# Optimization experiments

Measured on AMD Instinct MI355X. Metric: run time of the kernel, lower is better.

Reference implementation:

```python
import jax, jax.numpy as jnp
import numpy as np
from jax import lax

N_QUBITS = 10
Q_DEPTH = 3


def setup_inputs():
    k = jax.random.split(jax.random.key(0), 12)
    B = 2048
    return {
        "x": jax.random.normal(k[0], (B, 1, 28, 28), jnp.float32),
        "conv1_w": jax.random.normal(k[1], (16, 1, 3, 3), jnp.float32) * 0.2,
        "conv1_b": jnp.zeros((16,), jnp.float32),
        "bn1_g": jnp.ones((16,), jnp.float32),
        "bn1_b": jnp.zeros((16,), jnp.float32),
        "conv2_w": jax.random.normal(k[2], (32, 16, 3, 3), jnp.float32) * 0.1,
        "conv2_b": jnp.zeros((32,), jnp.float32),
        "bn2_g": jnp.ones((32,), jnp.float32),
        "bn2_b": jnp.zeros((32,), jnp.float32),
        "fc1_w": jax.random.normal(k[3], (784, 1568), jnp.float32) * 0.01,
        "fc1_b": jnp.zeros((784,), jnp.float32),
        "sel_w": jax.random.normal(k[4], (N_QUBITS, 784), jnp.float32) * 0.01,
        "sel_b": jnp.zeros((N_QUBITS,), jnp.float32),
        "q_params": 0.5 * jax.random.normal(k[5], (Q_DEPTH, N_QUBITS), jnp.float32),
        "post1_w": jax.random.normal(k[6], (32, N_QUBITS), jnp.float32) * 0.01,
        "post1_b": jnp.zeros((32,), jnp.float32),
        "post2_w": jax.random.normal(k[7], (10, 32), jnp.float32) * 0.01,
        "post2_b": jnp.zeros((10,), jnp.float32),
    }


def _conv(x, w, b):
    y = lax.conv_general_dilated(x, w, (1, 1), "SAME",
                                 dimension_numbers=("NCHW", "OIHW", "NCHW"))
    return y + b[None, :, None, None]


def _bn(x, g, b, eps=1e-5):
    # training-mode batch norm (batch statistics), as in the torch module's forward
    m = x.mean((0, 2, 3), keepdims=True)
    v = ((x - m) ** 2).mean((0, 2, 3), keepdims=True)
    return g[None, :, None, None] * (x - m) * lax.rsqrt(v + eps) + b[None, :, None, None]


def _maxpool2(x):
    return lax.reduce_window(x, -jnp.inf, lax.max, (1, 1, 2, 2), (1, 1, 2, 2), "VALID")


def _apply_ry(state, theta, wire):
    # state: real statevector shaped (2,)*N_QUBITS (RY/CZ keep amplitudes real)
    st = jnp.moveaxis(state, wire, 0)
    c, s = jnp.cos(theta / 2), jnp.sin(theta / 2)
    new = jnp.stack([c * st[0] - s * st[1], s * st[0] + c * st[1]])
    return jnp.moveaxis(new, 0, wire)


def _apply_cz(state, wire):
    st = jnp.moveaxis(state, (wire, wire + 1), (0, 1))
    st = st.at[1, 1].multiply(-1.0)
    return jnp.moveaxis(st, (0, 1), (wire, wire + 1))


def _circuit(feats, qw):
    # angle encoding + q_depth x (RY layer, linear CZ chain); returns <Z_i> per qubit
    state = jnp.zeros((2,) * N_QUBITS, feats.dtype).at[(0,) * N_QUBITS].set(1.0)
    for i in range(N_QUBITS):
        state = _apply_ry(state, feats[i] * jnp.pi, i)
    for layer in range(Q_DEPTH):
        for i in range(N_QUBITS):
            state = _apply_ry(state, qw[layer, i], i)
        for i in range(N_QUBITS - 1):
            state = _apply_cz(state, i)
    probs = state * state
    zs = []
    for i in range(N_QUBITS):
        p = jnp.moveaxis(probs, i, 0).reshape(2, -1).sum(1)
        zs.append(p[0] - p[1])
    return jnp.stack(zs)


def reference(x, conv1_w, conv1_b, bn1_g, bn1_b, conv2_w, conv2_b, bn2_g, bn2_b,
              fc1_w, fc1_b, sel_w, sel_b, q_params, post1_w, post1_b, post2_w, post2_b):
    h = _maxpool2(jax.nn.relu(_bn(_conv(x, conv1_w, conv1_b), bn1_g, bn1_b)))   # [B,16,14,14]
    h = _maxpool2(jax.nn.relu(_bn(_conv(h, conv2_w, conv2_b), bn2_g, bn2_b)))   # [B,32,7,7]
    h = h.reshape(h.shape[0], -1)                                               # [B,1568]
    feats = jnp.tanh(h @ fc1_w.T + fc1_b)                                       # [B,784]
    sel = feats @ sel_w.T + sel_b                                               # [B,10]
    q_out = jax.vmap(_circuit, in_axes=(0, None))(sel, q_params)                # [B,10]
    h2 = jax.nn.relu(q_out @ post1_w.T + post1_b)
    return h2 @ post2_w.T + post2_b
```

## Files before the change

kernel.cpp:

```cpp
#include <hip/hip_runtime.h>
#include <math.h>


#define BATCH 2048
#define PI_F 3.14159265358979323846f
#define KP 3328
#define KQ 13
#define BSTR2 312
#define AROW 392
#define APLANE 6272
#define AIMG 12544

typedef unsigned short ushort_t;
typedef __attribute__((ext_vector_type(8))) short bf16x8;
typedef __attribute__((ext_vector_type(4))) float f32x4;

__device__ __forceinline__ float wave_reduce_add(float v) {
#pragma unroll
  for (int off = 32; off >= 1; off >>= 1) v += __shfl_xor(v, off, 64);
  return v;
}

__device__ __forceinline__ ushort_t f2bf(float v) {
  unsigned u = __float_as_uint(v);
  u += 0x7FFFu + ((u >> 16) & 1u);
  return (ushort_t)(u >> 16);
}
__device__ __forceinline__ float bf2f(ushort_t b) {
  return __uint_as_float(((unsigned)b) << 16);
}

__device__ __forceinline__ float tanh_fast(float x) {
  float e = __expf(-2.f * fabsf(x));
  float r = (1.f - e) / (1.f + e);
  return copysignf(r, x);
}

__global__ __launch_bounds__(256) void k_conv1_stats(
    const float* __restrict__ x, const float* __restrict__ cw,
    const float* __restrict__ cb, float* __restrict__ part1,
    const float* __restrict__ cw2, ushort_t* __restrict__ wB,
    const float* __restrict__ fc1w, ushort_t* __restrict__ Bp) {
  const int t = threadIdx.x;
  if (blockIdx.x >= BATCH) {
    const int bid = blockIdx.x - BATCH;
    if (bid == 0) {
      for (int i = t; i < 32 * BSTR2; i += 256) {
        int oc = i / BSTR2, k = i - oc * BSTR2;
        ushort_t val = 0;
        if (k < 288) {
          int sec2 = k >> 4, ic = k & 15;
          if (sec2 < 9) {
            val = f2bf(cw2[oc * 144 + ic * 9 + sec2]);
          } else {
            float w = cw2[oc * 144 + ic * 9 + (sec2 - 9)];
            val = f2bf(w - bf2f(f2bf(w)));
          }
        }
        wB[i] = val;
      }
    } else {
      const int rb = (bid - 1) * 8;
      for (int i = t; i < 8 * (KP / 8); i += 256) {
        int rr = i / (KP / 8), c = i - rr * (KP / 8);
        int n = rb + rr;
        union { ushort_t u[8]; uint4 v; } o;
        o.v = make_uint4(0, 0, 0, 0);
        if (n < 784 && c < 392) {
          int cc = c < 196 ? c : c - 196;
          const float* wp = fc1w + (size_t)n * 1568 + cc * 8;
#pragma unroll
          for (int j = 0; j < 8; ++j) o.u[j] = f2bf(wp[j]);
        }
        ((uint4*)(Bp + (size_t)n * KP))[c] = o.v;
      }
    }
    return;
  }
  const int b = blockIdx.x;
  __shared__ float xs[30][33];
  __shared__ float ws[160];
  __shared__ float redS[16][28];
  __shared__ float redQ[16][28];
  for (int i = t; i < 30 * 33; i += 256) (&xs[0][0])[i] = 0.f;
  if (t < 144) ws[t] = cw[t];
  else if (t < 160) ws[t] = cb[t - 144];
  __syncthreads();
  const float* xb = x + b * 784;
  for (int i = t; i < 784; i += 256) xs[1 + i / 28][1 + (i % 28)] = xb[i];
  __syncthreads();
  for (int task = t; task < 448; task += 256) {
    const int oc = task / 28;
    const int row = task - oc * 28;
    float wk[9];
#pragma unroll
    for (int k = 0; k < 9; ++k) wk[k] = ws[oc * 9 + k];
    const float bc = ws[144 + oc];
    float A0 = xs[row][0], A1 = xs[row][1];
    float B0 = xs[row + 1][0], B1 = xs[row + 1][1];
    float C0 = xs[row + 2][0], C1 = xs[row + 2][1];
    float s = 0.f, q = 0.f;
#pragma unroll 4
    for (int xx = 0; xx < 28; ++xx) {
      float A2 = xs[row][xx + 2], B2 = xs[row + 1][xx + 2], C2 = xs[row + 2][xx + 2];
      float acc = bc;
      acc = fmaf(wk[0], A0, acc); acc = fmaf(wk[1], A1, acc); acc = fmaf(wk[2], A2, acc);
      acc = fmaf(wk[3], B0, acc); acc = fmaf(wk[4], B1, acc); acc = fmaf(wk[5], B2, acc);
      acc = fmaf(wk[6], C0, acc); acc = fmaf(wk[7], C1, acc); acc = fmaf(wk[8], C2, acc);
      s += acc; q = fmaf(acc, acc, q);
      A0 = A1; A1 = A2; B0 = B1; B1 = B2; C0 = C1; C1 = C2;
    }
    redS[oc][row] = s;
    redQ[oc][row] = q;
  }
  __syncthreads();
  if (t < 32) {
    const int c = t >> 1;
    float acc = 0.f;
    if (t & 1) {
#pragma unroll 4
      for (int r = 0; r < 28; ++r) acc += redQ[c][r];
    } else {
#pragma unroll 4
      for (int r = 0; r < 28; ++r) acc += redS[c][r];
    }
    part1[b * 32 + t] = acc;
  }
}

__global__ __launch_bounds__(256) void k_bnstat(
    const float* __restrict__ part, const float* __restrict__ g,
    const float* __restrict__ bb, float* __restrict__ stats,
    int nch, int nblk, double invN) {
  const int c = blockIdx.x;
  const int t = threadIdx.x;
  const int stride = nch * 2;
  double ls = 0.0, lq = 0.0;
  for (int i = t; i < nblk; i += 256) {
    ls += (double)part[i * stride + c * 2];
    lq += (double)part[i * stride + c * 2 + 1];
  }
#pragma unroll
  for (int off = 32; off >= 1; off >>= 1) {
    ls += __shfl_xor(ls, off, 64);
    lq += __shfl_xor(lq, off, 64);
  }
  __shared__ double rs[4], rq[4];
  if ((t & 63) == 0) { rs[t >> 6] = ls; rq[t >> 6] = lq; }
  __syncthreads();
  if (t == 0) {
    double S = rs[0] + rs[1] + rs[2] + rs[3];
    double Q = rq[0] + rq[1] + rq[2] + rq[3];
    double mean = S * invN;
    double var = Q * invN - mean * mean;
    double inv = 1.0 / sqrt(var + 1e-5);
    double sc = (double)g[c] * inv;
    stats[c * 2] = (float)sc;
    stats[c * 2 + 1] = (float)((double)bb[c] - mean * sc);
  }
}

__global__ __launch_bounds__(512, 2) void k_conv2_mfma(
    const float* __restrict__ x, const float* __restrict__ cw1,
    const float* __restrict__ cb1, const float* __restrict__ stats1,
    const ushort_t* __restrict__ wB, const float* __restrict__ cb,
    const float* __restrict__ g2, float* __restrict__ part2,
    float* __restrict__ pooled) {
  const int b0 = blockIdx.x * 2;
  const int t = threadIdx.x;
  __shared__ __align__(16) ushort_t aT[2 * AIMG];
  __shared__ __align__(16) ushort_t bS[32 * BSTR2];
  __shared__ float xs[2][30][33];
  __shared__ float wsc[160];
  __shared__ float red[2][4][64];
  {
    uint4 z = make_uint4(0, 0, 0, 0);
    uint4* a4 = (uint4*)aT;
    for (int i = t; i < (2 * AIMG) / 8; i += 512) a4[i] = z;
    float4* xz = (float4*)&xs[0][0][0];
    if (t < 495) xz[t] = make_float4(0.f, 0.f, 0.f, 0.f);
    if (t < 160) wsc[t] = (t < 144) ? cw1[t] : cb1[t - 144];
    uint4* b4 = (uint4*)bS;
    const uint4* w4 = (const uint4*)wB;
    for (int i = t; i < (32 * BSTR2) / 8; i += 512) b4[i] = w4[i];
  }
  __syncthreads();
  {
    const float* xb = x + (size_t)b0 * 784;
    for (int i = t; i < 1568; i += 512) {
      int img = i / 784, j = i - img * 784;
      xs[img][1 + j / 28][1 + (j % 28)] = xb[img * 784 + j];
    }
  }
  __syncthreads();
  if (t < 448) {
    const int img = t / 224, tt = t - img * 224;
    const int oc = tt / 14, pr = tt - oc * 14;
    float wk[9];
#pragma unroll
    for (int k = 0; k < 9; ++k) wk[k] = wsc[oc * 9 + k];
    const float bc = wsc[144 + oc];
    const float scale = stats1[oc * 2], shift = stats1[oc * 2 + 1];
    const int r0 = 2 * pr;
    float A0 = xs[img][r0][0],     A1 = xs[img][r0][1];
    float B0 = xs[img][r0 + 1][0], B1 = xs[img][r0 + 1][1];
    float C0 = xs[img][r0 + 2][0], C1 = xs[img][r0 + 2][1];
    float D0 = xs[img][r0 + 3][0], D1 = xs[img][r0 + 3][1];
    float pmax = 0.f;
#pragma unroll 4
    for (int xx = 0; xx < 28; ++xx) {
      float A2 = xs[img][r0][xx + 2], B2 = xs[img][r0 + 1][xx + 2];
      float C2 = xs[img][r0 + 2][xx + 2], D2 = xs[img][r0 + 3][xx + 2];
      float c0 = bc, c1 = bc;
      c0 = fmaf(wk[0], A0, c0); c0 = fmaf(wk[1], A1, c0); c0 = fmaf(wk[2], A2, c0);
      c0 = fmaf(wk[3], B0, c0); c0 = fmaf(wk[4], B1, c0); c0 = fmaf(wk[5], B2, c0);
      c0 = fmaf(wk[6], C0, c0); c0 = fmaf(wk[7], C1, c0); c0 = fmaf(wk[8], C2, c0);
      c1 = fmaf(wk[0], B0, c1); c1 = fmaf(wk[1], B1, c1); c1 = fmaf(wk[2], B2, c1);
      c1 = fmaf(wk[3], C0, c1); c1 = fmaf(wk[4], C1, c1); c1 = fmaf(wk[5], C2, c1);
      c1 = fmaf(wk[6], D0, c1); c1 = fmaf(wk[7], D1, c1); c1 = fmaf(wk[8], D2, c1);
      float e0 = fmaxf(fmaf(scale, c0, shift), 0.f);
      float e1 = fmaxf(fmaf(scale, c1, shift), 0.f);
      float m = fmaxf(e0, e1);
      if ((xx & 1) == 0) {
        pmax = m;
      } else {
        float pv = fmaxf(pmax, m);
        ushort_t hi = f2bf(pv);
        ushort_t lo = f2bf(pv - bf2f(hi));
        int off = img * AIMG + (pr + 1) * AROW + ((xx >> 1) + 1) * 24 + oc;
        aT[off] = hi;
        aT[off + APLANE] = lo;
      }
      A0 = A1; A1 = A2; B0 = B1; B1 = B2; C0 = C1; C1 = C2; D0 = D1; D1 = D2;
    }
  }
  __syncthreads();

  const int lane = t & 63;
  const int wv = t >> 6;
  const int img = wv >> 2, wi = wv & 3;
  const int ic0 = ((lane >> 4) & 1) * 8;
  const int hb = lane >> 5;
  const int imgbase = img * AIMG;
  int abase[4];
#pragma unroll
  for (int fi = 0; fi < 4; ++fi) {
    int f = wi + fi * 4;
    int pp = f * 16 + (lane & 15);
    int quad = pp >> 2;
    if (quad > 48) quad = 48;
    int corner = pp & 3;
    int qy = quad / 7, qx = quad - qy * 7;
    int y = 2 * qy + (corner >> 1), xq = 2 * qx + (corner & 1);
    abase[fi] = imgbase + y * AROW + xq * 24 + ic0;
  }
  f32x4 acc[4][2];
  {
    const float bias0 = cb[lane & 15];
    const float bias1 = cb[16 + (lane & 15)];
#pragma unroll
    for (int fi = 0; fi < 4; ++fi) {
      acc[fi][0] = (f32x4){bias0, bias0, bias0, bias0};
      acc[fi][1] = (f32x4){bias1, bias1, bias1, bias1};
    }
  }
  const int brow = (lane & 15) * BSTR2 + ic0;
#pragma unroll
  for (int kt = 0; kt < 14; ++kt) {
    int sec = 2 * kt + hb;
    int ss = sec >= 18 ? sec - 18 : (sec >= 9 ? sec - 9 : sec);
    int col16;
    if (sec >= 27) { ss = 8; col16 = 18; }
    else if (sec >= 18) col16 = 9 + ss;
    else col16 = ss;
    int plane = (sec >= 9 && sec < 18) ? 1 : 0;
    bf16x8 bv0 = *(const bf16x8*)&bS[brow + col16 * 16];
    bf16x8 bv1 = *(const bf16x8*)&bS[brow + 16 * BSTR2 + col16 * 16];
    int dy = ss / 3, dx = ss - dy * 3;
    int doff = plane * APLANE + dy * AROW + dx * 24;
#pragma unroll
    for (int fi = 0; fi < 4; ++fi) {
      if (wi + fi * 4 < 13) {
        bf16x8 av = *(const bf16x8*)&aT[doff + abase[fi]];
        acc[fi][0] = __builtin_amdgcn_mfma_f32_16x16x32_bf16(av, bv0, acc[fi][0], 0, 0, 0);
        acc[fi][1] = __builtin_amdgcn_mfma_f32_16x16x32_bf16(av, bv1, acc[fi][1], 0, 0, 0);
      }
    }
  }
  const float gs0 = g2[lane & 15];
  const float gs1 = g2[16 + (lane & 15)];
  float s0 = 0.f, q0 = 0.f, s1 = 0.f, q1 = 0.f;
  float* pm = pooled + (size_t)(b0 + img) * 1568;
#pragma unroll
  for (int fi = 0; fi < 4; ++fi) {
    int f = wi + fi * 4;
    int quad = f * 4 + (lane >> 4);
    if (quad < 49) {
      f32x4 a0 = acc[fi][0], a1 = acc[fi][1];
#pragma unroll
      for (int r = 0; r < 4; ++r) {
        s0 += a0[r]; q0 = fmaf(a0[r], a0[r], q0);
        s1 += a1[r]; q1 = fmaf(a1[r], a1[r], q1);
      }
      float mx0 = fmaxf(fmaxf(a0[0], a0[1]), fmaxf(a0[2], a0[3]));
      float mn0 = fminf(fminf(a0[0], a0[1]), fminf(a0[2], a0[3]));
      float mx1 = fmaxf(fmaxf(a1[0], a1[1]), fmaxf(a1[2], a1[3]));
      float mn1 = fminf(fminf(a1[0], a1[1]), fminf(a1[2], a1[3]));
      pm[quad * 32 + (lane & 15)] = (gs0 >= 0.f) ? mx0 : mn0;
      pm[quad * 32 + 16 + (lane & 15)] = (gs1 >= 0.f) ? mx1 : mn1;
    }
  }
  s0 += __shfl_xor(s0, 16, 64); s0 += __shfl_xor(s0, 32, 64);
  q0 += __shfl_xor(q0, 16, 64); q0 += __shfl_xor(q0, 32, 64);
  s1 += __shfl_xor(s1, 16, 64); s1 += __shfl_xor(s1, 32, 64);
  q1 += __shfl_xor(q1, 16, 64); q1 += __shfl_xor(q1, 32, 64);
  if (lane < 16) {
    red[img][wi][lane * 2] = s0;        red[img][wi][lane * 2 + 1] = q0;
    red[img][wi][(lane + 16) * 2] = s1; red[img][wi][(lane + 16) * 2 + 1] = q1;
  }
  __syncthreads();
  if (t < 128) {
    int im = t >> 6, c = t & 63;
    part2[(b0 + im) * 64 + c] =
        red[im][0][c] + red[im][1][c] + red[im][2][c] + red[im][3][c];
  }
}

__global__ __launch_bounds__(256) void k_pack_a(
    const float* __restrict__ pooled, const float* __restrict__ stats2,
    ushort_t* __restrict__ Ap) {
  const int m = blockIdx.x, t = threadIdx.x;
  __shared__ float rL[49 * 33];
  __shared__ float hv[1568];
  {
    const float4* src = (const float4*)(pooled + (size_t)m * 1568);
    for (int i = t; i < 392; i += 256) {
      int quad = i >> 3, oc4 = (i & 7) * 4;
      float4 v = src[i];
      float* d = &rL[quad * 33 + oc4];
      d[0] = v.x; d[1] = v.y; d[2] = v.z; d[3] = v.w;
    }
  }
  __syncthreads();
  for (int i = t; i < 1568; i += 256) {
    int oc = i / 49, quad = i - oc * 49;
    float val = rL[quad * 33 + oc];
    hv[i] = fmaxf(fmaf(stats2[oc * 2], val, stats2[oc * 2 + 1]), 0.f);
  }
  __syncthreads();
  ushort_t* ap = Ap + (size_t)m * KP;
  for (int c = t; c < KP / 8; c += 256) {
    union { ushort_t u[8]; uint4 v; } o;
    if (c < 196) {
#pragma unroll
      for (int j = 0; j < 8; ++j) o.u[j] = f2bf(hv[c * 8 + j]);
    } else if (c < 392) {
#pragma unroll
      for (int j = 0; j < 8; ++j) {
        float v = hv[(c - 196) * 8 + j];
        o.u[j] = f2bf(v - bf2f(f2bf(v)));
      }
    } else {
      o.v = make_uint4(0, 0, 0, 0);
    }
    *(uint4*)(ap + c * 8) = o.v;
  }
}

__global__ __launch_bounds__(512, 2) void k_fc1_mfma(
    const ushort_t* __restrict__ Ap, const ushort_t* __restrict__ Bp,
    float* __restrict__ partial) {
  __shared__ ushort_t As[128 * 64];
  __shared__ ushort_t Bs[128 * 64];
  const int t = threadIdx.x;
  const int id = blockIdx.x;
  const int xcd = id & 7, w = id >> 3;
  const int mtl = w / 28, rem = w - mtl * 28;
  const int ks = rem / 7, nt = rem - ks * 7;
  const int mt = xcd * 2 + mtl;
  const int m0 = mt * 128, n0 = nt * 128;
  const int lane = t & 63, wid = t >> 6;
  const int wm = wid >> 2, wn = wid & 3;

  const int srow = t >> 3, sslot = t & 7;
  const int xsl = (sslot ^ (srow & 7)) << 3;
  ushort_t* awp = &As[srow * 64 + xsl];
  ushort_t* bwp = &Bs[srow * 64 + xsl];
  const uint4* agp = (const uint4*)(Ap + (size_t)(m0 + srow) * KP) + sslot;
  const uint4* bgp = (const uint4*)(Bp + (size_t)(n0 + srow) * KP) + sslot;
  const int ROWOFF = 64 * (KP / 8);

  const int rbaseA = (wm * 64 + (lane & 15)) * 64;
  const int rbaseB = (wn * 32 + (lane & 15)) * 64;
  const int x0 = ((lane >> 4) ^ (lane & 7)) << 3;
  const int x1 = (((lane >> 4) + 4) ^ (lane & 7)) << 3;

  f32x4 acc[4][2];
#pragma unroll
  for (int fm = 0; fm < 4; ++fm) {
    acc[fm][0] = (f32x4){0.f, 0.f, 0.f, 0.f};
    acc[fm][1] = (f32x4){0.f, 0.f, 0.f, 0.f};
  }
  const int kt0 = ks * KQ;
  uint4 ca0 = agp[kt0 * 8], ca1 = agp[kt0 * 8 + ROWOFF];
  uint4 cb0 = bgp[kt0 * 8], cb1 = bgp[kt0 * 8 + ROWOFF];
  for (int kt = kt0; kt < kt0 + KQ; ++kt) {
    __syncthreads();
    *(uint4*)awp = ca0; *(uint4*)(awp + 64 * 64) = ca1;
    *(uint4*)bwp = cb0; *(uint4*)(bwp + 64 * 64) = cb1;
    __syncthreads();
    if (kt + 1 < kt0 + KQ) {
      ca0 = agp[(kt + 1) * 8]; ca1 = agp[(kt + 1) * 8 + ROWOFF];
      cb0 = bgp[(kt + 1) * 8]; cb1 = bgp[(kt + 1) * 8 + ROWOFF];
    }
#pragma unroll
    for (int kh = 0; kh < 2; ++kh) {
      const int xx = kh ? x1 : x0;
      bf16x8 b0 = *(const bf16x8*)&Bs[rbaseB + xx];
      bf16x8 b1 = *(const bf16x8*)&Bs[rbaseB + 16 * 64 + xx];
#pragma unroll
      for (int fm = 0; fm < 4; ++fm) {
        bf16x8 a = *(const bf16x8*)&As[rbaseA + fm * 1024 + xx];
        acc[fm][0] = __builtin_amdgcn_mfma_f32_16x16x32_bf16(a, b0, acc[fm][0], 0, 0, 0);
        acc[fm][1] = __builtin_amdgcn_mfma_f32_16x16x32_bf16(a, b1, acc[fm][1], 0, 0, 0);
      }
    }
  }
  const int mrow0 = m0 + wm * 64 + ((lane >> 4) << 2);
  const int col0 = n0 + wn * 32 + (lane & 15);
#pragma unroll
  for (int fm = 0; fm < 4; ++fm) {
#pragma unroll
    for (int fn = 0; fn < 2; ++fn) {
      int col = col0 + fn * 16;
      if (col < 832) {
        float* pb = partial + ((size_t)ks * 2048 + mrow0 + fm * 16) * 832 + col;
#pragma unroll
        for (int r = 0; r < 4; ++r) pb[(size_t)r * 832] = acc[fm][fn][r];
      }
    }
  }
}

template <int W>
__device__ __forceinline__ void ry_cs(float (&a)[16], int lane, float c, float s) {
  if (W < 4) {
    const int st = 1 << W;
#pragma unroll
    for (int r = 0; r < 16; ++r) {
      if (!(r & st)) {
        float lo = a[r], hi = a[r + st];
        a[r] = fmaf(c, lo, -s * hi);
        a[r + st] = fmaf(s, lo, c * hi);
      }
    }
  } else {
    const int m = 1 << (W - 4);
    const float sg = (lane & m) ? s : -s;
#pragma unroll
    for (int r = 0; r < 16; ++r) {
      float other = __shfl_xor(a[r], m, 64);
      a[r] = fmaf(c, a[r], sg * other);
    }
  }
}

#define RYCS(GC, GS)                                                  \
  {                                                                   \
    ry_cs<0>(a, lane, GC(0), GS(0)); ry_cs<1>(a, lane, GC(1), GS(1)); \
    ry_cs<2>(a, lane, GC(2), GS(2)); ry_cs<3>(a, lane, GC(3), GS(3)); \
    ry_cs<4>(a, lane, GC(4), GS(4)); ry_cs<5>(a, lane, GC(5), GS(5)); \
    ry_cs<6>(a, lane, GC(6), GS(6)); ry_cs<7>(a, lane, GC(7), GS(7)); \
    ry_cs<8>(a, lane, GC(8), GS(8)); ry_cs<9>(a, lane, GC(9), GS(9)); \
  }

__global__ __launch_bounds__(256) void k_tail(
    const float* __restrict__ partial, const float* __restrict__ fb,
    const float* __restrict__ sw, const float* __restrict__ sb,
    const float* __restrict__ qp, const float* __restrict__ w1,
    const float* __restrict__ b1, const float* __restrict__ w2,
    const float* __restrict__ b2, float* __restrict__ out) {
  const int t = threadIdx.x;
  __shared__ __align__(16) float swL[7840];
  __shared__ float lc[30], ls[30];
  __shared__ float hbuf[4][32];
  {
    const float4* swg = (const float4*)sw;
    float4* swd = (float4*)swL;
    for (int i = t; i < 1960; i += 256) swd[i] = swg[i];
  }
  if (t < 30) {
    float th = 0.5f * qp[t];
    lc[t] = __cosf(th);
    ls[t] = __sinf(th);
  }
  __syncthreads();
  const int wv = t >> 6;
  const int m = blockIdx.x * 4 + wv;
  const int lane = t & 63;

  const float4* p4 = (const float4*)(partial + (size_t)m * 832);
  const size_t KSL4 = (size_t)2048 * 832 / 4;
  const float4* fb4 = (const float4*)fb;
  const float4* sw4 = (const float4*)swL;
  float acc[10];
#pragma unroll
  for (int i = 0; i < 10; ++i) acc[i] = 0.f;
  for (int c4 = lane; c4 < 196; c4 += 64) {
    float4 v0 = p4[c4];
    float4 v1 = p4[c4 + KSL4];
    float4 v2 = p4[c4 + 2 * KSL4];
    float4 v3 = p4[c4 + 3 * KSL4];
    float4 bb = fb4[c4];
    float t0 = tanh_fast(v0.x + v1.x + v2.x + v3.x + bb.x);
    float t1 = tanh_fast(v0.y + v1.y + v2.y + v3.y + bb.y);
    float t2 = tanh_fast(v0.z + v1.z + v2.z + v3.z + bb.z);
    float t3 = tanh_fast(v0.w + v1.w + v2.w + v3.w + bb.w);
#pragma unroll
    for (int i = 0; i < 10; ++i) {
      float4 w = sw4[i * 196 + c4];
      acc[i] = fmaf(t0, w.x, acc[i]);
      acc[i] = fmaf(t1, w.y, acc[i]);
      acc[i] = fmaf(t2, w.z, acc[i]);
      acc[i] = fmaf(t3, w.w, acc[i]);
    }
  }
#pragma unroll
  for (int i = 0; i < 10; ++i) acc[i] = wave_reduce_add(acc[i]) + sb[i];

  float pc[10], psn[10];
#pragma unroll
  for (int i = 0; i < 10; ++i) {
    float h = fmaf(acc[i], 0.5f * PI_F, 0.5f * qp[i]);
    pc[i] = __cosf(h);
    psn[i] = __sinf(h);
  }
  float p01[4] = {pc[0] * pc[1], psn[0] * pc[1], pc[0] * psn[1], psn[0] * psn[1]};
  float p23[4] = {pc[2] * pc[3], psn[2] * pc[3], pc[2] * psn[3], psn[2] * psn[3]};
  float L = (lane & 1) ? psn[4] : pc[4];
  L *= ((lane >> 1) & 1) ? psn[5] : pc[5];
  L *= ((lane >> 2) & 1) ? psn[6] : pc[6];
  L *= ((lane >> 3) & 1) ? psn[7] : pc[7];
  L *= ((lane >> 4) & 1) ? psn[8] : pc[8];
  L *= ((lane >> 5) & 1) ? psn[9] : pc[9];
  float a[16];
#pragma unroll
  for (int r = 0; r < 16; ++r) a[r] = L * p01[r & 3] * p23[r >> 2];

  float czs[16];
#pragma unroll
  for (int r = 0; r < 16; ++r) {
    int idx = (lane << 4) | r;
    czs[r] = (__popc(idx & (idx >> 1)) & 1) ? -1.f : 1.f;
  }
#pragma unroll
  for (int r = 0; r < 16; ++r) a[r] *= czs[r];
#pragma unroll
  for (int layer = 1; layer < 3; ++layer) {
    const int lb = layer * 10;
#define LC(i) (lc[lb + i])
#define LS(i) (ls[lb + i])
    RYCS(LC, LS)
#undef LC
#undef LS
#pragma unroll
    for (int r = 0; r < 16; ++r) a[r] *= czs[r];
  }
  float p[16];
  float lt = 0.f;
#pragma unroll
  for (int r = 0; r < 16; ++r) { p[r] = a[r] * a[r]; lt += p[r]; }
  float z[10];
#pragma unroll
  for (int ww = 0; ww < 4; ++ww) {
    float v = 0.f;
#pragma unroll
    for (int r = 0; r < 16; ++r) v += ((r >> ww) & 1) ? -p[r] : p[r];
    z[ww] = v;
  }
#pragma unroll
  for (int ww = 4; ww < 10; ++ww) z[ww] = ((lane >> (ww - 4)) & 1) ? -lt : lt;
#pragma unroll
  for (int ww = 0; ww < 10; ++ww) z[ww] = wave_reduce_add(z[ww]);

  if (lane < 32) {
    float s = b1[lane];
#pragma unroll
    for (int i = 0; i < 10; ++i) s = fmaf(w1[lane * 10 + i], z[i], s);
    hbuf[wv][lane] = fmaxf(s, 0.f);
  }
  __syncthreads();
  if (lane < 10) {
    float s = b2[lane];
#pragma unroll
    for (int jj = 0; jj < 32; ++jj) s = fmaf(w2[lane * 32 + jj], hbuf[wv][jj], s);
    out[m * 10 + lane] = s;
  }
}

extern "C" void kernel_launch(void* const* d_in, const int* in_sizes, int n_in,
                              void* d_out, int out_size, void* d_ws, size_t ws_size,
                              hipStream_t stream) {
  (void)in_sizes; (void)n_in; (void)out_size; (void)ws_size;
  const float* x    = (const float*)d_in[0];
  const float* c1w  = (const float*)d_in[1];
  const float* c1b  = (const float*)d_in[2];
  const float* bn1g = (const float*)d_in[3];
  const float* bn1b = (const float*)d_in[4];
  const float* c2w  = (const float*)d_in[5];
  const float* c2b  = (const float*)d_in[6];
  const float* bn2g = (const float*)d_in[7];
  const float* bn2b = (const float*)d_in[8];
  const float* fc1w = (const float*)d_in[9];
  const float* fc1b = (const float*)d_in[10];
  const float* selw = (const float*)d_in[11];
  const float* selb = (const float*)d_in[12];
  const float* qpar = (const float*)d_in[13];
  const float* p1w  = (const float*)d_in[14];
  const float* p1b  = (const float*)d_in[15];
  const float* p2w  = (const float*)d_in[16];
  const float* p2b  = (const float*)d_in[17];

  float* ws = (float*)d_ws;
  ushort_t* Ap = (ushort_t*)ws;
  size_t o = 6422528;
  float* pooled  = ws + o;
  float* partial = ws + o;
  o += 6815744;
  ushort_t* Bp  = (ushort_t*)(ws + o); o += 1490944;
  ushort_t* wB  = (ushort_t*)(ws + o); o += 4992;
  float* part1  = ws + o; o += 65536;
  float* part2  = ws + o; o += 131072;
  float* stats1 = ws + o; o += 32;
  float* stats2 = ws + o; o += 64;
  float* outp   = (float*)d_out;

  k_conv1_stats<<<BATCH + 1 + 112, 256, 0, stream>>>(x, c1w, c1b, part1, c2w,
                                                     wB, fc1w, Bp);
  k_bnstat<<<16, 256, 0, stream>>>(part1, bn1g, bn1b, stats1, 16, BATCH,
                                   1.0 / (2048.0 * 784.0));
  k_conv2_mfma<<<BATCH / 2, 512, 0, stream>>>(x, c1w, c1b, stats1, wB, c2b,
                                              bn2g, part2, pooled);
  k_bnstat<<<32, 256, 0, stream>>>(part2, bn2g, bn2b, stats2, 32, BATCH,
                                   1.0 / (2048.0 * 196.0));
  k_pack_a<<<BATCH, 256, 0, stream>>>(pooled, stats2, Ap);
  k_fc1_mfma<<<448, 512, 0, stream>>>(Ap, Bp, partial);
  k_tail<<<BATCH / 4, 256, 0, stream>>>(partial, fc1b, selw, selb, qpar,
                                        p1w, p1b, p2w, p2b, outp);
}
```

Baseline: 103.5 us.

## Interleave fc1 split-K partials per row and split tail reduction across two waves

The fc1 MFMA kernel now writes its four split-K partial results interleaved per row, so the tail kernel reads one contiguous 3328-float row instead of four slices far apart. The tail kernel doubles to 512 threads, with two waves sharing each batch row's feature reduction. Their partial sums are combined through shared memory with an extra barrier. Half the waves then sit idle during the quantum-circuit and MLP part, trading added synchronisation for more parallelism in the memory-bound reduction.

```diff
diff --git a/kernel.cpp b/kernel.cpp
--- a/kernel.cpp
+++ b/kernel.cpp
@@ -434,9 +434,9 @@
     for (int fn = 0; fn < 2; ++fn) {
       int col = col0 + fn * 16;
       if (col < 832) {
-        float* pb = partial + ((size_t)ks * 2048 + mrow0 + fm * 16) * 832 + col;
-#pragma unroll
-        for (int r = 0; r < 4; ++r) pb[(size_t)r * 832] = acc[fm][fn][r];
+        float* pb = partial + ((size_t)(mrow0 + fm * 16) * 4 + ks) * 832 + col;
+#pragma unroll
+        for (int r = 0; r < 4; ++r) pb[(size_t)r * 4 * 832] = acc[fm][fn][r];
       }
     }
   }
@@ -474,7 +474,7 @@
     ry_cs<8>(a, lane, GC(8), GS(8)); ry_cs<9>(a, lane, GC(9), GS(9)); \
   }
 
-__global__ __launch_bounds__(256) void k_tail(
+__global__ __launch_bounds__(512) void k_tail(
     const float* __restrict__ partial, const float* __restrict__ fb,
     const float* __restrict__ sw, const float* __restrict__ sb,
     const float* __restrict__ qp, const float* __restrict__ w1,
@@ -484,10 +484,11 @@
   __shared__ __align__(16) float swL[7840];
   __shared__ float lc[30], ls[30];
   __shared__ float hbuf[4][32];
+  __shared__ float psum[8][12];
   {
     const float4* swg = (const float4*)sw;
     float4* swd = (float4*)swL;
-    for (int i = t; i < 1960; i += 256) swd[i] = swg[i];
+    for (int i = t; i < 1960; i += 512) swd[i] = swg[i];
   }
   if (t < 30) {
     float th = 0.5f * qp[t];
@@ -496,21 +497,22 @@
   }
   __syncthreads();
   const int wv = t >> 6;
-  const int m = blockIdx.x * 4 + wv;
   const int lane = t & 63;
-
-  const float4* p4 = (const float4*)(partial + (size_t)m * 832);
-  const size_t KSL4 = (size_t)2048 * 832 / 4;
+  const int r = wv >> 1;
+  const int half = wv & 1;
+  const int m = blockIdx.x * 4 + r;
+
+  const float4* p4 = (const float4*)(partial + (size_t)m * 3328);
   const float4* fb4 = (const float4*)fb;
   const float4* sw4 = (const float4*)swL;
   float acc[10];
 #pragma unroll
   for (int i = 0; i < 10; ++i) acc[i] = 0.f;
-  for (int c4 = lane; c4 < 196; c4 += 64) {
+  for (int c4 = lane + half * 64; c4 < 196; c4 += 128) {
     float4 v0 = p4[c4];
-    float4 v1 = p4[c4 + KSL4];
-    float4 v2 = p4[c4 + 2 * KSL4];
-    float4 v3 = p4[c4 + 3 * KSL4];
+    float4 v1 = p4[c4 + 208];
+    float4 v2 = p4[c4 + 416];
+    float4 v3 = p4[c4 + 624];
     float4 bb = fb4[c4];
     float t0 = tanh_fast(v0.x + v1.x + v2.x + v3.x + bb.x);
     float t1 = tanh_fast(v0.y + v1.y + v2.y + v3.y + bb.y);
@@ -526,74 +528,85 @@
     }
   }
 #pragma unroll
-  for (int i = 0; i < 10; ++i) acc[i] = wave_reduce_add(acc[i]) + sb[i];
-
-  float pc[10], psn[10];
-#pragma unroll
-  for (int i = 0; i < 10; ++i) {
-    float h = fmaf(acc[i], 0.5f * PI_F, 0.5f * qp[i]);
-    pc[i] = __cosf(h);
-    psn[i] = __sinf(h);
-  }
-  float p01[4] = {pc[0] * pc[1], psn[0] * pc[1], pc[0] * psn[1], psn[0] * psn[1]};
-  float p23[4] = {pc[2] * pc[3], psn[2] * pc[3], pc[2] * psn[3], psn[2] * psn[3]};
-  float L = (lane & 1) ? psn[4] : pc[4];
-  L *= ((lane >> 1) & 1) ? psn[5] : pc[5];
-  L *= ((lane >> 2) & 1) ? psn[6] : pc[6];
-  L *= ((lane >> 3) & 1) ? psn[7] : pc[7];
-  L *= ((lane >> 4) & 1) ? psn[8] : pc[8];
-  L *= ((lane >> 5) & 1) ? psn[9] : pc[9];
-  float a[16];
-#pragma unroll
-  for (int r = 0; r < 16; ++r) a[r] = L * p01[r & 3] * p23[r >> 2];
-
-  float czs[16];
-#pragma unroll
-  for (int r = 0; r < 16; ++r) {
-    int idx = (lane << 4) | r;
-    czs[r] = (__popc(idx & (idx >> 1)) & 1) ? -1.f : 1.f;
-  }
-#pragma unroll
-  for (int r = 0; r < 16; ++r) a[r] *= czs[r];
-#pragma unroll
-  for (int layer = 1; layer < 3; ++layer) {
-    const int lb = layer * 10;
+  for (int i = 0; i < 10; ++i) acc[i] = wave_reduce_add(acc[i]);
+  if (lane == 0) {
+#pragma unroll
+    for (int i = 0; i < 10; ++i) psum[wv][i] = acc[i];
+  }
+  __syncthreads();
+
+  if (half == 0) {
+#pragma unroll
+    for (int i = 0; i < 10; ++i)
+      acc[i] = psum[wv][i] + psum[wv + 1][i] + sb[i];
+
+    float pc[10], psn[10];
+#pragma unroll
+    for (int i = 0; i < 10; ++i) {
+      float h = fmaf(acc[i], 0.5f * PI_F, 0.5f * qp[i]);
+      pc[i] = __cosf(h);
+      psn[i] = __sinf(h);
+    }
+    float p01[4] = {pc[0] * pc[1], psn[0] * pc[1], pc[0] * psn[1], psn[0] * psn[1]};
+    float p23[4] = {pc[2] * pc[3], psn[2] * pc[3], pc[2] * psn[3], psn[2] * psn[3]};
+    float L = (lane & 1) ? psn[4] : pc[4];
+    L *= ((lane >> 1) & 1) ? psn[5] : pc[5];
+    L *= ((lane >> 2) & 1) ? psn[6] : pc[6];
+    L *= ((lane >> 3) & 1) ? psn[7] : pc[7];
+    L *= ((lane >> 4) & 1) ? psn[8] : pc[8];
+    L *= ((lane >> 5) & 1) ? psn[9] : pc[9];
+    float a[16];
+#pragma unroll
+    for (int rr = 0; rr < 16; ++rr) a[rr] = L * p01[rr & 3] * p23[rr >> 2];
+
+    float czs[16];
+#pragma unroll
+    for (int rr = 0; rr < 16; ++rr) {
+      int idx = (lane << 4) | rr;
+      czs[rr] = (__popc(idx & (idx >> 1)) & 1) ? -1.f : 1.f;
+    }
+#pragma unroll
+    for (int rr = 0; rr < 16; ++rr) a[rr] *= czs[rr];
+#pragma unroll
+    for (int layer = 1; layer < 3; ++layer) {
+      const int lb = layer * 10;
 #define LC(i) (lc[lb + i])
 #define LS(i) (ls[lb + i])
-    RYCS(LC, LS)
+      RYCS(LC, LS)
 #undef LC
 #undef LS
 #pragma unroll
-    for (int r = 0; r < 16; ++r) a[r] *= czs[r];
-  }
-  float p[16];
-  float lt = 0.f;
-#pragma unroll
-  for (int r = 0; r < 16; ++r) { p[r] = a[r] * a[r]; lt += p[r]; }
-  float z[10];
-#pragma unroll
-  for (int ww = 0; ww < 4; ++ww) {
-    float v = 0.f;
-#pragma unroll
-    for (int r = 0; r < 16; ++r) v += ((r >> ww) & 1) ? -p[r] : p[r];
-    z[ww] = v;
-  }
-#pragma unroll
-  for (int ww = 4; ww < 10; ++ww) z[ww] = ((lane >> (ww - 4)) & 1) ? -lt : lt;
-#pragma unroll
-  for (int ww = 0; ww < 10; ++ww) z[ww] = wave_reduce_add(z[ww]);
-
-  if (lane < 32) {
-    float s = b1[lane];
-#pragma unroll
-    for (int i = 0; i < 10; ++i) s = fmaf(w1[lane * 10 + i], z[i], s);
-    hbuf[wv][lane] = fmaxf(s, 0.f);
-  }
-  __syncthreads();
-  if (lane < 10) {
+      for (int rr = 0; rr < 16; ++rr) a[rr] *= czs[rr];
+    }
+    float p[16];
+    float lt = 0.f;
+#pragma unroll
+    for (int rr = 0; rr < 16; ++rr) { p[rr] = a[rr] * a[rr]; lt += p[rr]; }
+    float z[10];
+#pragma unroll
+    for (int ww = 0; ww < 4; ++ww) {
+      float v = 0.f;
+#pragma unroll
+      for (int rr = 0; rr < 16; ++rr) v += ((rr >> ww) & 1) ? -p[rr] : p[rr];
+      z[ww] = v;
+    }
+#pragma unroll
+    for (int ww = 4; ww < 10; ++ww) z[ww] = ((lane >> (ww - 4)) & 1) ? -lt : lt;
+#pragma unroll
+    for (int ww = 0; ww < 10; ++ww) z[ww] = wave_reduce_add(z[ww]);
+
+    if (lane < 32) {
+      float s = b1[lane];
+#pragma unroll
+      for (int i = 0; i < 10; ++i) s = fmaf(w1[lane * 10 + i], z[i], s);
+      hbuf[r][lane] = fmaxf(s, 0.f);
+    }
+  }
+  __syncthreads();
+  if (half == 0 && lane < 10) {
     float s = b2[lane];
 #pragma unroll
-    for (int jj = 0; jj < 32; ++jj) s = fmaf(w2[lane * 32 + jj], hbuf[wv][jj], s);
+    for (int jj = 0; jj < 32; ++jj) s = fmaf(w2[lane * 32 + jj], hbuf[r][jj], s);
     out[m * 10 + lane] = s;
   }
 }
@@ -645,6 +658,6 @@
                                    1.0 / (2048.0 * 196.0));
   k_pack_a<<<BATCH, 256, 0, stream>>>(pooled, stats2, Ap);
   k_fc1_mfma<<<448, 512, 0, stream>>>(Ap, Bp, partial);
-  k_tail<<<BATCH / 4, 256, 0, stream>>>(partial, fc1b, selw, selb, qpar,
+  k_tail<<<BATCH / 4, 512, 0, stream>>>(partial, fc1b, selw, selb, qpar,
                                         p1w, p1b, p2w, p2b, outp);
 }
```

New measurement: 106.7 us. +3.1%, slower.

## Fuse BN2/ReLU/bf16 split packing into fc1 MFMA A-tile load

Applied to the files above, without the earlier changes.

Removes the separate k_pack_a kernel. The fc1 GEMM now reads pooled fp32 activations directly, applies the BN2 affine transform and ReLU, and produces the bf16 hi/lo split on the fly while staging A tiles into shared memory. The pooled layout is changed to channel-major so each K chunk maps onto contiguous floats. This saves one launch and a write-plus-read of the packed A matrix, at the cost of extra ALU work and doubled fp32 loads inside the GEMM loop. The last K split is shortened to skip the zero padding.

```diff
diff --git a/kernel.cpp b/kernel.cpp
--- a/kernel.cpp
+++ b/kernel.cpp
@@ -5,7 +5,6 @@
 #define BATCH 2048
 #define PI_F 3.14159265358979323846f
 #define KP 3328
-#define KQ 13
 #define BSTR2 312
 #define AROW 392
 #define APLANE 6272
@@ -34,6 +33,20 @@
   float e = __expf(-2.f * fabsf(x));
   float r = (1.f - e) / (1.f + e);
   return copysignf(r, x);
+}
+
+__device__ __forceinline__ uint4 xformA(float4 fa, float4 fb, int i0, bool lo,
+                                        const float* __restrict__ st2) {
+  float f[8] = {fa.x, fa.y, fa.z, fa.w, fb.x, fb.y, fb.z, fb.w};
+  union { ushort_t u[8]; uint4 v; } o;
+#pragma unroll
+  for (int j = 0; j < 8; ++j) {
+    int oc = ((i0 + j) * 1338) >> 16;
+    float hv = fmaxf(fmaf(st2[oc * 2], f[j], st2[oc * 2 + 1]), 0.f);
+    ushort_t hi = f2bf(hv);
+    o.u[j] = lo ? f2bf(hv - bf2f(hi)) : hi;
+  }
+  return o.v;
 }
 
 __global__ __launch_bounds__(256) void k_conv1_stats(
@@ -306,8 +319,8 @@
       float mn0 = fminf(fminf(a0[0], a0[1]), fminf(a0[2], a0[3]));
       float mx1 = fmaxf(fmaxf(a1[0], a1[1]), fmaxf(a1[2], a1[3]));
       float mn1 = fminf(fminf(a1[0], a1[1]), fminf(a1[2], a1[3]));
-      pm[quad * 32 + (lane & 15)] = (gs0 >= 0.f) ? mx0 : mn0;
-      pm[quad * 32 + 16 + (lane & 15)] = (gs1 >= 0.f) ? mx1 : mn1;
+      pm[(lane & 15) * 49 + quad] = (gs0 >= 0.f) ? mx0 : mn0;
+      pm[(16 + (lane & 15)) * 49 + quad] = (gs1 >= 0.f) ? mx1 : mn1;
     }
   }
   s0 += __shfl_xor(s0, 16, 64); s0 += __shfl_xor(s0, 32, 64);
@@ -326,53 +339,14 @@
   }
 }
 
-__global__ __launch_bounds__(256) void k_pack_a(
+__global__ __launch_bounds__(512, 2) void k_fc1_mfma(
     const float* __restrict__ pooled, const float* __restrict__ stats2,
-    ushort_t* __restrict__ Ap) {
-  const int m = blockIdx.x, t = threadIdx.x;
-  __shared__ float rL[49 * 33];
-  __shared__ float hv[1568];
-  {
-    const float4* src = (const float4*)(pooled + (size_t)m * 1568);
-    for (int i = t; i < 392; i += 256) {
-      int quad = i >> 3, oc4 = (i & 7) * 4;
-      float4 v = src[i];
-      float* d = &rL[quad * 33 + oc4];
-      d[0] = v.x; d[1] = v.y; d[2] = v.z; d[3] = v.w;
-    }
-  }
-  __syncthreads();
-  for (int i = t; i < 1568; i += 256) {
-    int oc = i / 49, quad = i - oc * 49;
-    float val = rL[quad * 33 + oc];
-    hv[i] = fmaxf(fmaf(stats2[oc * 2], val, stats2[oc * 2 + 1]), 0.f);
-  }
-  __syncthreads();
-  ushort_t* ap = Ap + (size_t)m * KP;
-  for (int c = t; c < KP / 8; c += 256) {
-    union { ushort_t u[8]; uint4 v; } o;
-    if (c < 196) {
-#pragma unroll
-      for (int j = 0; j < 8; ++j) o.u[j] = f2bf(hv[c * 8 + j]);
-    } else if (c < 392) {
-#pragma unroll
-      for (int j = 0; j < 8; ++j) {
-        float v = hv[(c - 196) * 8 + j];
-        o.u[j] = f2bf(v - bf2f(f2bf(v)));
-      }
-    } else {
-      o.v = make_uint4(0, 0, 0, 0);
-    }
-    *(uint4*)(ap + c * 8) = o.v;
-  }
-}
-
-__global__ __launch_bounds__(512, 2) void k_fc1_mfma(
-    const ushort_t* __restrict__ Ap, const ushort_t* __restrict__ Bp,
-    float* __restrict__ partial) {
+    const ushort_t* __restrict__ Bp, float* __restrict__ partial) {
   __shared__ ushort_t As[128 * 64];
   __shared__ ushort_t Bs[128 * 64];
+  __shared__ float st2[64];
   const int t = threadIdx.x;
+  if (t < 64) st2[t] = stats2[t];
   const int id = blockIdx.x;
   const int xcd = id & 7, w = id >> 3;
   const int mtl = w / 28, rem = w - mtl * 28;
@@ -386,7 +360,8 @@
   const int xsl = (sslot ^ (srow & 7)) << 3;
   ushort_t* awp = &As[srow * 64 + xsl];
   ushort_t* bwp = &Bs[srow * 64 + xsl];
-  const uint4* agp = (const uint4*)(Ap + (size_t)(m0 + srow) * KP) + sslot;
+  const float* prow0 = pooled + (size_t)(m0 + srow) * 1568;
+  const float* prow1 = prow0 + (size_t)64 * 1568;
   const uint4* bgp = (const uint4*)(Bp + (size_t)(n0 + srow) * KP) + sslot;
   const int ROWOFF = 64 * (KP / 8);
 
@@ -401,17 +376,40 @@
     acc[fm][0] = (f32x4){0.f, 0.f, 0.f, 0.f};
     acc[fm][1] = (f32x4){0.f, 0.f, 0.f, 0.f};
   }
-  const int kt0 = ks * KQ;
-  uint4 ca0 = agp[kt0 * 8], ca1 = agp[kt0 * 8 + ROWOFF];
-  uint4 cb0 = bgp[kt0 * 8], cb1 = bgp[kt0 * 8 + ROWOFF];
-  for (int kt = kt0; kt < kt0 + KQ; ++kt) {
+  const int kt0 = ks * 13;
+  const int ktEnd = (ks == 3) ? 49 : kt0 + 13;
+
+  float4 fa00, fa01, fa10, fa11;
+  uint4 cb0, cb1;
+  {
+    int c = kt0 * 64 + sslot * 8;
+    int ci = (c < 1568) ? c : c - 1568;
+    fa00 = *(const float4*)(prow0 + ci);
+    fa01 = *(const float4*)(prow0 + ci + 4);
+    fa10 = *(const float4*)(prow1 + ci);
+    fa11 = *(const float4*)(prow1 + ci + 4);
+    cb0 = bgp[kt0 * 8];
+    cb1 = bgp[kt0 * 8 + ROWOFF];
+  }
+  for (int kt = kt0; kt < ktEnd; ++kt) {
+    const int c = kt * 64 + sslot * 8;
+    const bool lo = c >= 1568;
+    const int i0 = lo ? c - 1568 : c;
     __syncthreads();
-    *(uint4*)awp = ca0; *(uint4*)(awp + 64 * 64) = ca1;
-    *(uint4*)bwp = cb0; *(uint4*)(bwp + 64 * 64) = cb1;
+    *(uint4*)awp = xformA(fa00, fa01, i0, lo, st2);
+    *(uint4*)(awp + 64 * 64) = xformA(fa10, fa11, i0, lo, st2);
+    *(uint4*)bwp = cb0;
+    *(uint4*)(bwp + 64 * 64) = cb1;
     __syncthreads();
-    if (kt + 1 < kt0 + KQ) {
-      ca0 = agp[(kt + 1) * 8]; ca1 = agp[(kt + 1) * 8 + ROWOFF];
-      cb0 = bgp[(kt + 1) * 8]; cb1 = bgp[(kt + 1) * 8 + ROWOFF];
+    if (kt + 1 < ktEnd) {
+      int cn = (kt + 1) * 64 + sslot * 8;
+      int cin = (cn < 1568) ? cn : cn - 1568;
+      fa00 = *(const float4*)(prow0 + cin);
+      fa01 = *(const float4*)(prow0 + cin + 4);
+      fa10 = *(const float4*)(prow1 + cin);
+      fa11 = *(const float4*)(prow1 + cin + 4);
+      cb0 = bgp[(kt + 1) * 8];
+      cb1 = bgp[(kt + 1) * 8 + ROWOFF];
     }
 #pragma unroll
     for (int kh = 0; kh < 2; ++kh) {
@@ -622,11 +620,9 @@
   const float* p2b  = (const float*)d_in[17];
 
   float* ws = (float*)d_ws;
-  ushort_t* Ap = (ushort_t*)ws;
-  size_t o = 6422528;
-  float* pooled  = ws + o;
-  float* partial = ws + o;
-  o += 6815744;
+  float* pooled  = ws;
+  size_t o = 3211264;
+  float* partial = ws + o; o += 6815744;
   ushort_t* Bp  = (ushort_t*)(ws + o); o += 1490944;
   ushort_t* wB  = (ushort_t*)(ws + o); o += 4992;
   float* part1  = ws + o; o += 65536;
@@ -643,8 +639,7 @@
                                               bn2g, part2, pooled);
   k_bnstat<<<32, 256, 0, stream>>>(part2, bn2g, bn2b, stats2, 32, BATCH,
                                    1.0 / (2048.0 * 196.0));
-  k_pack_a<<<BATCH, 256, 0, stream>>>(pooled, stats2, Ap);
-  k_fc1_mfma<<<448, 512, 0, stream>>>(Ap, Bp, partial);
+  k_fc1_mfma<<<448, 512, 0, stream>>>(pooled, stats2, Bp, partial);
   k_tail<<<BATCH / 4, 256, 0, stream>>>(partial, fc1b, selw, selb, qpar,
                                         p1w, p1b, p2w, p2b, outp);
 }
```

New measurement: 106.8 us. 3.2% more time.
